# Kernel tuning notes

Hardware: AMD Instinct MI355X
Metric: run time of the kernel (lower is better)

The kernel has to match this reference:

```python
import math
import jax, jax.numpy as jnp
import numpy as np

B, N, D, H = 2, 2048, 1024, 16
HD = D // H  # 64
TWO_PI = 2.0 * math.pi
ROPE_BASE = 10000.0


def setup_inputs() -> dict:
    key = jax.random.key(0)
    ks = jax.random.split(key, 8)
    s = 0.02
    x = jax.random.normal(ks[0], (B, N, D), dtype=jnp.float32)
    Wq = jax.random.normal(ks[1], (D, D), dtype=jnp.float32) * s
    Wk = jax.random.normal(ks[2], (D, D), dtype=jnp.float32) * s
    Wv = jax.random.normal(ks[3], (D, D), dtype=jnp.float32) * s
    Wo = jax.random.normal(ks[4], (D, D), dtype=jnp.float32) * s
    cw = jax.random.normal(ks[5], (D,), dtype=jnp.float32) * s  # complexity_proj weight
    cb = jnp.zeros((), dtype=jnp.float32)                        # complexity_proj bias
    alpha = jnp.asarray(0.1, dtype=jnp.float32)
    T_base = jnp.asarray(10.0, dtype=jnp.float32)
    root_ids = jax.random.randint(ks[6], (B, N), 0, 1000)
    mask = jnp.tril(jnp.ones((N, N), dtype=jnp.int32))  # causal
    return {"x": x, "Wq": Wq, "Wk": Wk, "Wv": Wv, "Wo": Wo,
            "alpha": alpha, "T_base": T_base, "cw": cw, "cb": cb,
            "root_ids": root_ids, "mask": mask, "t_step": 3}


def _rope_cos_sin(seq_len, head_dim, dtype):
    inv_freq = 1.0 / (ROPE_BASE ** (jnp.arange(0, head_dim, 2, dtype=jnp.float32) / head_dim))
    pos = jnp.arange(seq_len, dtype=jnp.float32)
    freqs = pos[:, None] * inv_freq[None, :]          # (N, HD/2)
    emb = jnp.concatenate([freqs, freqs], axis=-1)    # (N, HD)
    return jnp.cos(emb).astype(dtype), jnp.sin(emb).astype(dtype)


def _rotate_half(t):
    half = t.shape[-1] // 2
    return jnp.concatenate([-t[..., half:], t[..., :half]], axis=-1)


def reference(x, Wq, Wk, Wv, Wo, alpha, T_base, cw, cb, root_ids, mask, t_step):
    b, n, d = x.shape
    # QKV projection -> (B, H, N, HD)
    def proj(W):
        return jnp.einsum('bnd,ed->bne', x, W).reshape(b, n, H, HD).transpose(0, 2, 1, 3)
    q, k, v = proj(Wq), proj(Wk), proj(Wv)
    # RoPE
    cos, sin = _rope_cos_sin(n, HD, x.dtype)          # (N, HD)
    q = q * cos + _rotate_half(q) * sin
    k = k * cos + _rotate_half(k) * sin
    # Per-sample temperature via complexity + cardiac oscillation
    complexity = jax.nn.sigmoid(jnp.einsum('bd,d->b', x.mean(axis=1), cw) + cb)  # (B,)
    T_eff = (jnp.abs(T_base) + 1.0) * (0.5 + complexity)                          # (B,)
    psi = 1.0 + alpha * jnp.sin(TWO_PI * t_step / T_eff)                          # (B,)
    scale = (math.sqrt(HD) * psi)[:, None, None, None]                            # (B,1,1,1)
    # Attention with full NxN scores (eager path, as in source)
    scores = jnp.einsum('bhqd,bhkd->bhqk', q, k) / scale
    scores = jnp.where(mask[None, None, :, :] == 0, -jnp.inf, scores)
    attn = jax.nn.softmax(scores, axis=-1)
    out = jnp.einsum('bhqk,bhkd->bhqd', attn, v)       # (B,H,N,HD)
    out = out.transpose(0, 2, 1, 3).reshape(b, n, d)
    return jnp.einsum('bnd,ed->bne', out, Wo)
```

## Files before the change

kernel.cpp:

```cpp
#include <hip/hip_runtime.h>


typedef short short8 __attribute__((ext_vector_type(8)));
typedef float floatx4 __attribute__((ext_vector_type(4)));
typedef float f32x16 __attribute__((ext_vector_type(16)));
typedef unsigned int uint4v __attribute__((ext_vector_type(4)));
typedef unsigned int u32x4v __attribute__((ext_vector_type(4)));
typedef unsigned short us4 __attribute__((ext_vector_type(4)));
typedef unsigned short u16;

#define DEV __device__ __forceinline__

static const int Bb = 2;

static const size_t OFF_XB = 0;
static const size_t OFF_WQ = 8388608;
static const size_t OFF_WK = OFF_WQ + 2097152;
static const size_t OFF_WV = OFF_WK + 2097152;
static const size_t OFF_WO = OFF_WV + 2097152;
static const size_t OFF_Q  = OFF_WO + 2097152;
static const size_t OFF_K  = OFF_Q + 8388608;
static const size_t OFF_V  = OFF_K + 8388608;
static const size_t OFF_AO = OFF_V + 8388608;
static const size_t OFF_SC = OFF_AO + 8388608;

DEV u16 f2bf(float f) {
  unsigned int u = __builtin_bit_cast(unsigned int, f);
  u += 0x7fffu + ((u >> 16) & 1u);
  return (u16)(u >> 16);
}

DEV unsigned pkbf(float lo, float hi) {
  unsigned r;
  asm("v_cvt_pk_bf16_f32 %0, %1, %2" : "=v"(r) : "v"(lo), "v"(hi));
  return r;
}

__global__ void cvt_kernel(const float* __restrict__ src, u16* __restrict__ dst, int n4) {
  int i = blockIdx.x * 256 + threadIdx.x;
  if (i >= n4) return;
  float4 f = ((const float4*)src)[i];
  us4 o;
  o[0] = f2bf(f.x); o[1] = f2bf(f.y); o[2] = f2bf(f.z); o[3] = f2bf(f.w);
  ((us4*)dst)[i] = o;
}

__global__ void scale_partial_kernel(const float* __restrict__ x,
                                     const float* __restrict__ cw,
                                     float* __restrict__ part) {
  int blk = blockIdx.x;
  int b = blk >> 6, sl = blk & 63;
  const float4* xp = (const float4*)(x + (size_t)b * 2097152) + (size_t)sl * 8192;
  float acc = 0.f;
  for (int i = threadIdx.x; i < 8192; i += 256) {
    float4 f = xp[i];
    int d4 = (sl * 8192 + i) & 255;
    float4 c = ((const float4*)cw)[d4];
    acc += f.x * c.x + f.y * c.y + f.z * c.z + f.w * c.w;
  }
  __shared__ float red[256];
  red[threadIdx.x] = acc;
  __syncthreads();
  for (int s = 128; s > 0; s >>= 1) {
    if (threadIdx.x < s) red[threadIdx.x] += red[threadIdx.x + s];
    __syncthreads();
  }
  if (threadIdx.x == 0) atomicAdd(&part[b], red[0]);
}

__global__ void scale_finalize_kernel(const float* __restrict__ part,
                                      const float* __restrict__ cb,
                                      const float* __restrict__ alpha,
                                      const float* __restrict__ tb,
                                      const int* __restrict__ tstep,
                                      float* __restrict__ out) {
  int b = threadIdx.x;
  if (b >= Bb) return;
  float sm = part[b] * (1.0f / 2048.0f) + cb[0];
  float cx = 1.0f / (1.0f + expf(-sm));
  float Te = (fabsf(tb[0]) + 1.0f) * (0.5f + cx);
  float psi = 1.0f + alpha[0] * sinf(6.283185307179586f * (float)tstep[0] / Te);
  out[b] = 1.0f / (8.0f * psi);
}

__global__ __launch_bounds__(256) void gemm_qkv_kernel(
    const u16* __restrict__ xb, const u16* __restrict__ wq, const u16* __restrict__ wk,
    const u16* __restrict__ wv, u16* __restrict__ q, u16* __restrict__ k,
    u16* __restrict__ v) {
  const int tm = blockIdx.x, tn = blockIdx.y, which = blockIdx.z;
  const u16* W = (which == 0) ? wq : (which == 1) ? wk : wv;
  u16* dst = (which == 0) ? q : (which == 1) ? k : v;

  __shared__ __align__(16) u16 As[128 * 32];
  __shared__ __align__(16) u16 Bs[128 * 32];

  const int t = threadIdx.x, lane = t & 63, w = t >> 6;
  const int wm = w >> 1, wn = w & 1, lg = lane >> 4, lr = lane & 15;

  floatx4 acc[4][4];
#pragma unroll
  for (int i = 0; i < 4; i++)
#pragma unroll
    for (int j = 0; j < 4; j++) acc[i][j] = (floatx4){0.f, 0.f, 0.f, 0.f};

  const int rowA = tm * 128, rowB = tn * 128;
  for (int kt = 0; kt < 32; ++kt) {
#pragma unroll
    for (int s = 0; s < 2; s++) {
      int c = t + s * 256;
      int r = c >> 2, kc = c & 3;
      *(uint4v*)(As + r * 32 + kc * 8) =
          *(const uint4v*)(xb + (size_t)(rowA + r) * 1024 + kt * 32 + kc * 8);
      *(uint4v*)(Bs + r * 32 + kc * 8) =
          *(const uint4v*)(W + (size_t)(rowB + r) * 1024 + kt * 32 + kc * 8);
    }
    __syncthreads();
    short8 af[4], bw[4];
#pragma unroll
    for (int i = 0; i < 4; i++)
      af[i] = *(const short8*)(As + (wm * 64 + i * 16 + lr) * 32 + lg * 8);
#pragma unroll
    for (int j = 0; j < 4; j++)
      bw[j] = *(const short8*)(Bs + (wn * 64 + j * 16 + lr) * 32 + lg * 8);
#pragma unroll
    for (int i = 0; i < 4; i++)
#pragma unroll
      for (int j = 0; j < 4; j++)
        acc[i][j] = __builtin_amdgcn_mfma_f32_16x16x32_bf16(af[i], bw[j], acc[i][j], 0, 0, 0);
    __syncthreads();
  }

  const int rowbase = tm * 128 + wm * 64, colbase = tn * 128 + wn * 64;
  if (which <= 1) {
#pragma unroll
    for (int i = 0; i < 4; i++)
#pragma unroll
      for (int ii = 0; ii < 4; ii++) {
        int gm = rowbase + i * 16 + lg * 4 + ii;
        int pos = gm & 2047, bb = gm >> 11;
#pragma unroll
        for (int jp = 0; jp < 2; jp++) {
          int hd2 = jp * 16 + lr;
          float ang = (float)pos * exp2f(-(float)hd2 * 0.41524101186092030f);
          float sv, cv;
          sincosf(ang, &sv, &cv);
          float a0 = acc[i][jp][ii], a1 = acc[i][jp + 2][ii];
          int e0 = colbase + jp * 16 + lr;
          int hh = e0 >> 6;
          size_t base = (((size_t)bb * 16 + hh) * 2048 + pos) * 64;
          dst[base + hd2]      = f2bf(a0 * cv - a1 * sv);
          dst[base + hd2 + 32] = f2bf(a1 * cv + a0 * sv);
        }
      }
  } else {
#pragma unroll
    for (int i = 0; i < 4; i++)
#pragma unroll
      for (int ii = 0; ii < 4; ii++) {
        int gm = rowbase + i * 16 + lg * 4 + ii;
        int pos = gm & 2047, bb = gm >> 11;
#pragma unroll
        for (int j = 0; j < 4; j++) {
          int ge = colbase + j * 16 + lr;
          int hh = ge >> 6, hd = ge & 63;
          dst[(((size_t)bb * 16 + hh) * 2048 + pos) * 64 + hd] = f2bf(acc[i][j][ii]);
        }
      }
  }
}

__global__ __launch_bounds__(256) void vtrans_kernel(const u16* __restrict__ v,
                                                     u16* __restrict__ vt) {
  const int bh = blockIdx.x, nt = blockIdx.y;
  __shared__ __align__(16) u16 T[64 * 64];
  const int t = threadIdx.x;
  const size_t vi = (size_t)bh * 131072 + (size_t)nt * 4096;
#pragma unroll
  for (int s = 0; s < 2; s++) {
    int g = s * 256 + t, n = g >> 3, dc = g & 7;
    *(uint4v*)(T + n * 64 + ((dc ^ (n & 7)) * 8)) =
        *(const uint4v*)(v + vi + (size_t)n * 64 + dc * 8);
  }
  __syncthreads();
  const size_t vo = (size_t)bh * 131072 + (size_t)nt * 64;
#pragma unroll
  for (int s = 0; s < 2; s++) {
    int g = s * 256 + t, nc = g & 7, d = g >> 3;
    short8 o;
#pragma unroll
    for (int jj = 0; jj < 8; jj++) {
      int n = nc * 8 + jj;
      o[jj] = (short)T[n * 64 + (((d >> 3) ^ (n & 7)) * 8) + (d & 7)];
    }
    *(short8*)(vt + vo + (size_t)d * 2048 + nc * 8) = o;
  }
}

__global__ __launch_bounds__(256) void attn_kernel(
    const u16* __restrict__ q, const u16* __restrict__ k, const u16* __restrict__ vt,
    u16* __restrict__ ao, const float* __restrict__ scale_ws) {
  const int bid = blockIdx.x;
  const int swz = (bid & 7) * 64 + (bid >> 3);
  const int bh = swz >> 4, p = swz & 15;
  const int b = bh >> 4, h = bh & 15;
  const int w = threadIdx.x >> 6, lane = threadIdx.x & 63;
  const int l31 = lane & 31, hi = lane >> 5;
  const int tsel = (w == 0) ? p : (w == 1) ? 31 - p : (w == 2) ? 32 + p : 63 - p;
  const int q0 = tsel * 32;
  const int KT = tsel >> 1;
  const float isc2 = scale_ws[b] * 1.4426950408889634f;
  const size_t koff = (size_t)bh * 131072;
  const float NINF = -__builtin_inff();

  short8 bq[4];
#pragma unroll
  for (int k4 = 0; k4 < 4; k4++)
    bq[k4] = *(const short8*)(q + koff + (size_t)(q0 + l31) * 64 + k4 * 16 + hi * 8);

  f32x16 o0, o1;
#pragma unroll
  for (int r = 0; r < 16; r++) { o0[r] = 0.f; o1[r] = 0.f; }
  float m2 = NINF, ell = 0.f;

  for (int kt = 0; kt <= KT; ++kt) {
    const int cbase = kt << 6;
    const bool haveMt1 = (cbase + 32 <= q0 + 31);

    short8 ka0[4], ka1[4];
#pragma unroll
    for (int k4 = 0; k4 < 4; k4++)
      ka0[k4] = *(const short8*)(k + koff + (size_t)(cbase + l31) * 64 + k4 * 16 + hi * 8);
    if (haveMt1) {
#pragma unroll
      for (int k4 = 0; k4 < 4; k4++)
        ka1[k4] = *(const short8*)(k + koff + (size_t)(cbase + 32 + l31) * 64 + k4 * 16 + hi * 8);
    }
    const int nct = haveMt1 ? 4 : 2;
    short8 va0[4], va1[4];
#pragma unroll
    for (int ct = 0; ct < 4; ct++) {
      if (ct < nct) {
        va0[ct] = *(const short8*)(vt + koff + (size_t)l31 * 2048 + cbase + ct * 16 + hi * 8);
        va1[ct] = *(const short8*)(vt + koff + (size_t)(32 + l31) * 2048 + cbase + ct * 16 + hi * 8);
      }
    }

    f32x16 s0, s1;
#pragma unroll
    for (int r = 0; r < 16; r++) { s0[r] = 0.f; s1[r] = 0.f; }
#pragma unroll
    for (int k4 = 0; k4 < 4; k4++)
      s0 = __builtin_amdgcn_mfma_f32_32x32x16_bf16(ka0[k4], bq[k4], s0, 0, 0, 0);
    if (haveMt1) {
#pragma unroll
      for (int k4 = 0; k4 < 4; k4++)
        s1 = __builtin_amdgcn_mfma_f32_32x32x16_bf16(ka1[k4], bq[k4], s1, 0, 0, 0);
    }

#pragma unroll
    for (int r = 0; r < 16; r++) { s0[r] *= isc2; s1[r] *= isc2; }
    if (kt == KT) {
      const int thr = q0 + l31 - cbase;
#pragma unroll
      for (int r = 0; r < 16; r++) {
        const int crow = (r & 3) + 8 * (r >> 2) + 4 * hi;
        if (crow > thr) s0[r] = NINF;
        if (crow + 32 > thr) s1[r] = NINF;
      }
    }

    float mx = s0[0];
#pragma unroll
    for (int r = 1; r < 16; r++) mx = fmaxf(mx, s0[r]);
#pragma unroll
    for (int r = 0; r < 16; r++) mx = fmaxf(mx, s1[r]);
    mx = fmaxf(mx, __shfl_xor(mx, 32, 64));
    const float mn = fmaxf(m2, mx);
    const float rsc = exp2f(m2 - mn);
    m2 = mn;
    f32x16 p0, p1;
    float ps = 0.f;
#pragma unroll
    for (int r = 0; r < 16; r++) { p0[r] = exp2f(s0[r] - mn); ps += p0[r]; }
#pragma unroll
    for (int r = 0; r < 16; r++) { p1[r] = exp2f(s1[r] - mn); ps += p1[r]; }
    ps += __shfl_xor(ps, 32, 64);
    ell = ell * rsc + ps;
#pragma unroll
    for (int r = 0; r < 16; r++) { o0[r] *= rsc; o1[r] *= rsc; }

#pragma unroll
    for (int ct = 0; ct < 4; ct++) {
      if (ct < nct) {
        const f32x16& pp = (ct < 2) ? p0 : p1;
        const int rA = (ct & 1) * 8;
        unsigned pkA0 = pkbf(pp[rA + 0], pp[rA + 1]);
        unsigned pkA1 = pkbf(pp[rA + 2], pp[rA + 3]);
        unsigned pkB0 = pkbf(pp[rA + 4], pp[rA + 5]);
        unsigned pkB1 = pkbf(pp[rA + 6], pp[rA + 7]);
        unsigned u0 = (unsigned)__shfl_xor((int)(hi ? pkA0 : pkB0), 32, 64);
        unsigned u1 = (unsigned)__shfl_xor((int)(hi ? pkA1 : pkB1), 32, 64);
        u32x4v pu;
        pu[0] = hi ? u0 : pkA0;
        pu[1] = hi ? u1 : pkA1;
        pu[2] = hi ? pkB0 : u0;
        pu[3] = hi ? pkB1 : u1;
        short8 pf = __builtin_bit_cast(short8, pu);
        o0 = __builtin_amdgcn_mfma_f32_32x32x16_bf16(va0[ct], pf, o0, 0, 0, 0);
        o1 = __builtin_amdgcn_mfma_f32_32x32x16_bf16(va1[ct], pf, o1, 0, 0, 0);
      }
    }
  }

  const float invl = 1.0f / ell;
  u16* orow = ao + ((size_t)(b * 2048 + q0 + l31)) * 1024 + h * 64;
#pragma unroll
  for (int qd = 0; qd < 4; qd++) {
    us4 st0, st1;
#pragma unroll
    for (int j = 0; j < 4; j++) {
      st0[j] = f2bf(o0[qd * 4 + j] * invl);
      st1[j] = f2bf(o1[qd * 4 + j] * invl);
    }
    *(us4*)(orow + qd * 8 + hi * 4) = st0;
    *(us4*)(orow + 32 + qd * 8 + hi * 4) = st1;
  }
}

__global__ __launch_bounds__(256) void gemm_out_kernel(const u16* __restrict__ ab,
                                                       const u16* __restrict__ wo,
                                                       float* __restrict__ out) {
  const int tm = blockIdx.x, tn = blockIdx.y;
  __shared__ __align__(16) u16 As[128 * 32];
  __shared__ __align__(16) u16 Bs[128 * 32];

  const int t = threadIdx.x, lane = t & 63, w = t >> 6;
  const int wm = w >> 1, wn = w & 1, lg = lane >> 4, lr = lane & 15;

  floatx4 acc[4][4];
#pragma unroll
  for (int i = 0; i < 4; i++)
#pragma unroll
    for (int j = 0; j < 4; j++) acc[i][j] = (floatx4){0.f, 0.f, 0.f, 0.f};

  const int rowA = tm * 128, rowB = tn * 128;
  for (int kt = 0; kt < 32; ++kt) {
#pragma unroll
    for (int s = 0; s < 2; s++) {
      int c = t + s * 256;
      int r = c >> 2, kc = c & 3;
      *(uint4v*)(As + r * 32 + kc * 8) =
          *(const uint4v*)(ab + (size_t)(rowA + r) * 1024 + kt * 32 + kc * 8);
      *(uint4v*)(Bs + r * 32 + kc * 8) =
          *(const uint4v*)(wo + (size_t)(rowB + r) * 1024 + kt * 32 + kc * 8);
    }
    __syncthreads();
    short8 af[4], bw[4];
#pragma unroll
    for (int i = 0; i < 4; i++)
      af[i] = *(const short8*)(As + (wm * 64 + i * 16 + lr) * 32 + lg * 8);
#pragma unroll
    for (int j = 0; j < 4; j++)
      bw[j] = *(const short8*)(Bs + (wn * 64 + j * 16 + lr) * 32 + lg * 8);
#pragma unroll
    for (int i = 0; i < 4; i++)
#pragma unroll
      for (int j = 0; j < 4; j++)
        acc[i][j] = __builtin_amdgcn_mfma_f32_16x16x32_bf16(af[i], bw[j], acc[i][j], 0, 0, 0);
    __syncthreads();
  }

  const int rowbase = tm * 128 + wm * 64, colbase = tn * 128 + wn * 64;
#pragma unroll
  for (int i = 0; i < 4; i++)
#pragma unroll
    for (int ii = 0; ii < 4; ii++) {
      int gm = rowbase + i * 16 + lg * 4 + ii;
#pragma unroll
      for (int j = 0; j < 4; j++) {
        int ge = colbase + j * 16 + lr;
        out[(size_t)gm * 1024 + ge] = acc[i][j][ii];
      }
    }
}

extern "C" void kernel_launch(void* const* d_in, const int* in_sizes, int n_in,
                              void* d_out, int out_size, void* d_ws, size_t ws_size,
                              hipStream_t stream) {
  const float* x     = (const float*)d_in[0];
  const float* Wq    = (const float*)d_in[1];
  const float* Wk    = (const float*)d_in[2];
  const float* Wv    = (const float*)d_in[3];
  const float* Wo    = (const float*)d_in[4];
  const float* alpha = (const float*)d_in[5];
  const float* Tb    = (const float*)d_in[6];
  const float* cw    = (const float*)d_in[7];
  const float* cb    = (const float*)d_in[8];
  const int*   tstep = (const int*)d_in[11];

  char* ws = (char*)d_ws;
  u16* xb  = (u16*)(ws + OFF_XB);
  u16* wqb = (u16*)(ws + OFF_WQ);
  u16* wkb = (u16*)(ws + OFF_WK);
  u16* wvb = (u16*)(ws + OFF_WV);
  u16* wob = (u16*)(ws + OFF_WO);
  u16* qb  = (u16*)(ws + OFF_Q);
  u16* kb  = (u16*)(ws + OFF_K);
  u16* vb  = (u16*)(ws + OFF_V);
  u16* aob = (u16*)(ws + OFF_AO);
  u16* vtb = (u16*)(ws + OFF_XB);
  float* sc = (float*)(ws + OFF_SC);

  cvt_kernel<<<4096, 256, 0, stream>>>(x, xb, 1048576);
  cvt_kernel<<<1024, 256, 0, stream>>>(Wq, wqb, 262144);
  cvt_kernel<<<1024, 256, 0, stream>>>(Wk, wkb, 262144);
  cvt_kernel<<<1024, 256, 0, stream>>>(Wv, wvb, 262144);
  cvt_kernel<<<1024, 256, 0, stream>>>(Wo, wob, 262144);

  hipMemsetAsync(sc + 2, 0, 2 * sizeof(float), stream);
  scale_partial_kernel<<<128, 256, 0, stream>>>(x, cw, sc + 2);
  scale_finalize_kernel<<<1, 64, 0, stream>>>(sc + 2, cb, alpha, Tb, tstep, sc);

  gemm_qkv_kernel<<<dim3(32, 8, 3), 256, 0, stream>>>(xb, wqb, wkb, wvb, qb, kb, vb);

  vtrans_kernel<<<dim3(32, 32), 256, 0, stream>>>(vb, vtb);

  attn_kernel<<<dim3(512), 256, 0, stream>>>(qb, kb, vtb, aob, sc);

  gemm_out_kernel<<<dim3(32, 8), 256, 0, stream>>>(aob, wob, (float*)d_out);
}
```

Baseline: 282.6 us.

## Fuse conversion kernels, precompute RoPE table, use direct global-to-LDS loads in GEMMs

Merges the five fp32-to-bf16 conversion launches and the complexity partial-sum reduction into a single kernel, so x is read once for both jobs and launch overhead drops. Adds a small kernel that precomputes the RoPE cos/sin table into workspace, replacing per-element sincosf in the QKV GEMM epilogue with a table lookup. Both GEMMs now stage tiles with global_load_lds 16-byte transfers instead of going through registers. The trade-off is a block-wide reduction plus atomic in every x-conversion block, one extra launch, and reliance on the attention-output buffer being free to hold the table before attention writes it.

```diff
diff --git a/kernel.cpp b/kernel.cpp
--- a/kernel.cpp
+++ b/kernel.cpp
@@ -10,6 +10,11 @@
 typedef unsigned short u16;
 
 #define DEV __device__ __forceinline__
+
+#define GLOAD16(g, l)                                                      \
+  __builtin_amdgcn_global_load_lds(                                        \
+      (const __attribute__((address_space(1))) void*)(g),                  \
+      (__attribute__((address_space(3))) void*)(l), 16, 0, 0)
 
 static const int Bb = 2;
 
@@ -36,36 +41,40 @@
   return r;
 }
 
-__global__ void cvt_kernel(const float* __restrict__ src, u16* __restrict__ dst, int n4) {
-  int i = blockIdx.x * 256 + threadIdx.x;
-  if (i >= n4) return;
-  float4 f = ((const float4*)src)[i];
-  us4 o;
-  o[0] = f2bf(f.x); o[1] = f2bf(f.y); o[2] = f2bf(f.z); o[3] = f2bf(f.w);
-  ((us4*)dst)[i] = o;
-}
-
-__global__ void scale_partial_kernel(const float* __restrict__ x,
-                                     const float* __restrict__ cw,
-                                     float* __restrict__ part) {
-  int blk = blockIdx.x;
-  int b = blk >> 6, sl = blk & 63;
-  const float4* xp = (const float4*)(x + (size_t)b * 2097152) + (size_t)sl * 8192;
-  float acc = 0.f;
-  for (int i = threadIdx.x; i < 8192; i += 256) {
-    float4 f = xp[i];
-    int d4 = (sl * 8192 + i) & 255;
-    float4 c = ((const float4*)cw)[d4];
-    acc += f.x * c.x + f.y * c.y + f.z * c.z + f.w * c.w;
-  }
-  __shared__ float red[256];
-  red[threadIdx.x] = acc;
-  __syncthreads();
-  for (int s = 128; s > 0; s >>= 1) {
-    if (threadIdx.x < s) red[threadIdx.x] += red[threadIdx.x + s];
+__global__ __launch_bounds__(256) void cvt_all_kernel(
+    const float* __restrict__ x, const float* __restrict__ wq,
+    const float* __restrict__ wk, const float* __restrict__ wv,
+    const float* __restrict__ wo, const float* __restrict__ cw,
+    u16* __restrict__ xb, u16* __restrict__ wqb, u16* __restrict__ wkb,
+    u16* __restrict__ wvb, u16* __restrict__ wob, float* __restrict__ part) {
+  const int blk = blockIdx.x;
+  if (blk < 4096) {
+    int i = blk * 256 + threadIdx.x;
+    float4 f = ((const float4*)x)[i];
+    us4 o;
+    o[0] = f2bf(f.x); o[1] = f2bf(f.y); o[2] = f2bf(f.z); o[3] = f2bf(f.w);
+    ((us4*)xb)[i] = o;
+    float4 c = ((const float4*)cw)[i & 255];
+    float acc = f.x * c.x + f.y * c.y + f.z * c.z + f.w * c.w;
+    __shared__ float red[256];
+    red[threadIdx.x] = acc;
     __syncthreads();
-  }
-  if (threadIdx.x == 0) atomicAdd(&part[b], red[0]);
+    for (int s = 128; s > 0; s >>= 1) {
+      if (threadIdx.x < s) red[threadIdx.x] += red[threadIdx.x + s];
+      __syncthreads();
+    }
+    if (threadIdx.x == 0) atomicAdd(&part[blk >> 11], red[0]);
+  } else {
+    int r = blk - 4096;
+    int wi = r >> 10;
+    int i = (r & 1023) * 256 + threadIdx.x;
+    const float* src = (wi == 0) ? wq : (wi == 1) ? wk : (wi == 2) ? wv : wo;
+    u16* dst = (wi == 0) ? wqb : (wi == 1) ? wkb : (wi == 2) ? wvb : wob;
+    float4 f = ((const float4*)src)[i];
+    us4 o;
+    o[0] = f2bf(f.x); o[1] = f2bf(f.y); o[2] = f2bf(f.z); o[3] = f2bf(f.w);
+    ((us4*)dst)[i] = o;
+  }
 }
 
 __global__ void scale_finalize_kernel(const float* __restrict__ part,
@@ -83,10 +92,19 @@
   out[b] = 1.0f / (8.0f * psi);
 }
 
+__global__ void rope_table_kernel(float2* __restrict__ rt) {
+  int i = blockIdx.x * 256 + threadIdx.x;
+  int pos = i >> 5, hd2 = i & 31;
+  float ang = (float)pos * exp2f(-(float)hd2 * 0.41524101186092030f);
+  float sv, cv;
+  sincosf(ang, &sv, &cv);
+  rt[i] = make_float2(cv, sv);
+}
+
 __global__ __launch_bounds__(256) void gemm_qkv_kernel(
     const u16* __restrict__ xb, const u16* __restrict__ wq, const u16* __restrict__ wk,
-    const u16* __restrict__ wv, u16* __restrict__ q, u16* __restrict__ k,
-    u16* __restrict__ v) {
+    const u16* __restrict__ wv, const float2* __restrict__ rt,
+    u16* __restrict__ q, u16* __restrict__ k, u16* __restrict__ v) {
   const int tm = blockIdx.x, tn = blockIdx.y, which = blockIdx.z;
   const u16* W = (which == 0) ? wq : (which == 1) ? wk : wv;
   u16* dst = (which == 0) ? q : (which == 1) ? k : v;
@@ -104,16 +122,16 @@
     for (int j = 0; j < 4; j++) acc[i][j] = (floatx4){0.f, 0.f, 0.f, 0.f};
 
   const int rowA = tm * 128, rowB = tn * 128;
+  const u16* gA = xb + (size_t)(rowA + w * 32 + (lane >> 2)) * 1024 + (lane & 3) * 8;
+  const u16* gB = W + (size_t)(rowB + w * 32 + (lane >> 2)) * 1024 + (lane & 3) * 8;
+  u16* lA = As + w * 1024;
+  u16* lB = Bs + w * 1024;
+
   for (int kt = 0; kt < 32; ++kt) {
-#pragma unroll
-    for (int s = 0; s < 2; s++) {
-      int c = t + s * 256;
-      int r = c >> 2, kc = c & 3;
-      *(uint4v*)(As + r * 32 + kc * 8) =
-          *(const uint4v*)(xb + (size_t)(rowA + r) * 1024 + kt * 32 + kc * 8);
-      *(uint4v*)(Bs + r * 32 + kc * 8) =
-          *(const uint4v*)(W + (size_t)(rowB + r) * 1024 + kt * 32 + kc * 8);
-    }
+    GLOAD16(gA, lA);
+    GLOAD16(gA + 16 * 1024, lA + 512);
+    GLOAD16(gB, lB);
+    GLOAD16(gB + 16 * 1024, lB + 512);
     __syncthreads();
     short8 af[4], bw[4];
 #pragma unroll
@@ -128,6 +146,7 @@
       for (int j = 0; j < 4; j++)
         acc[i][j] = __builtin_amdgcn_mfma_f32_16x16x32_bf16(af[i], bw[j], acc[i][j], 0, 0, 0);
     __syncthreads();
+    gA += 32; gB += 32;
   }
 
   const int rowbase = tm * 128 + wm * 64, colbase = tn * 128 + wn * 64;
@@ -141,15 +160,13 @@
 #pragma unroll
         for (int jp = 0; jp < 2; jp++) {
           int hd2 = jp * 16 + lr;
-          float ang = (float)pos * exp2f(-(float)hd2 * 0.41524101186092030f);
-          float sv, cv;
-          sincosf(ang, &sv, &cv);
+          float2 cs = rt[pos * 32 + hd2];
           float a0 = acc[i][jp][ii], a1 = acc[i][jp + 2][ii];
           int e0 = colbase + jp * 16 + lr;
           int hh = e0 >> 6;
           size_t base = (((size_t)bb * 16 + hh) * 2048 + pos) * 64;
-          dst[base + hd2]      = f2bf(a0 * cv - a1 * sv);
-          dst[base + hd2 + 32] = f2bf(a1 * cv + a0 * sv);
+          dst[base + hd2]      = f2bf(a0 * cs.x - a1 * cs.y);
+          dst[base + hd2 + 32] = f2bf(a1 * cs.x + a0 * cs.y);
         }
       }
   } else {
@@ -344,16 +361,16 @@
     for (int j = 0; j < 4; j++) acc[i][j] = (floatx4){0.f, 0.f, 0.f, 0.f};
 
   const int rowA = tm * 128, rowB = tn * 128;
+  const u16* gA = ab + (size_t)(rowA + w * 32 + (lane >> 2)) * 1024 + (lane & 3) * 8;
+  const u16* gB = wo + (size_t)(rowB + w * 32 + (lane >> 2)) * 1024 + (lane & 3) * 8;
+  u16* lA = As + w * 1024;
+  u16* lB = Bs + w * 1024;
+
   for (int kt = 0; kt < 32; ++kt) {
-#pragma unroll
-    for (int s = 0; s < 2; s++) {
-      int c = t + s * 256;
-      int r = c >> 2, kc = c & 3;
-      *(uint4v*)(As + r * 32 + kc * 8) =
-          *(const uint4v*)(ab + (size_t)(rowA + r) * 1024 + kt * 32 + kc * 8);
-      *(uint4v*)(Bs + r * 32 + kc * 8) =
-          *(const uint4v*)(wo + (size_t)(rowB + r) * 1024 + kt * 32 + kc * 8);
-    }
+    GLOAD16(gA, lA);
+    GLOAD16(gA + 16 * 1024, lA + 512);
+    GLOAD16(gB, lB);
+    GLOAD16(gB + 16 * 1024, lB + 512);
     __syncthreads();
     short8 af[4], bw[4];
 #pragma unroll
@@ -368,6 +385,7 @@
       for (int j = 0; j < 4; j++)
         acc[i][j] = __builtin_amdgcn_mfma_f32_16x16x32_bf16(af[i], bw[j], acc[i][j], 0, 0, 0);
     __syncthreads();
+    gA += 32; gB += 32;
   }
 
   const int rowbase = tm * 128 + wm * 64, colbase = tn * 128 + wn * 64;
@@ -409,19 +427,17 @@
   u16* vb  = (u16*)(ws + OFF_V);
   u16* aob = (u16*)(ws + OFF_AO);
   u16* vtb = (u16*)(ws + OFF_XB);
+  float2* rt = (float2*)(ws + OFF_AO);
   float* sc = (float*)(ws + OFF_SC);
 
-  cvt_kernel<<<4096, 256, 0, stream>>>(x, xb, 1048576);
-  cvt_kernel<<<1024, 256, 0, stream>>>(Wq, wqb, 262144);
-  cvt_kernel<<<1024, 256, 0, stream>>>(Wk, wkb, 262144);
-  cvt_kernel<<<1024, 256, 0, stream>>>(Wv, wvb, 262144);
-  cvt_kernel<<<1024, 256, 0, stream>>>(Wo, wob, 262144);
-
   hipMemsetAsync(sc + 2, 0, 2 * sizeof(float), stream);
-  scale_partial_kernel<<<128, 256, 0, stream>>>(x, cw, sc + 2);
+
+  cvt_all_kernel<<<8192, 256, 0, stream>>>(x, Wq, Wk, Wv, Wo, cw,
+                                           xb, wqb, wkb, wvb, wob, sc + 2);
   scale_finalize_kernel<<<1, 64, 0, stream>>>(sc + 2, cb, alpha, Tb, tstep, sc);
-
-  gemm_qkv_kernel<<<dim3(32, 8, 3), 256, 0, stream>>>(xb, wqb, wkb, wvb, qb, kb, vb);
+  rope_table_kernel<<<256, 256, 0, stream>>>(rt);
+
+  gemm_qkv_kernel<<<dim3(32, 8, 3), 256, 0, stream>>>(xb, wqb, wkb, wvb, rt, qb, kb, vb);
 
   vtrans_kernel<<<dim3(32, 32), 256, 0, stream>>>(vb, vtb);
 
```

New measurement: 307.0 us. +8.6%, slower.
